# Kernel tuning notes

Hardware: AMD Instinct MI355X
Metric: run time of the kernel (lower is better)

Reference implementation:

```python
import jax, jax.numpy as jnp
import numpy as np

N = 100000   # nodes
E = 1600000  # edges (avg degree 16)
D = 128      # in_dim == hidden_dim
L = 3        # num_layers
LN_EPS = 1e-5


def setup_inputs() -> dict:
    key = jax.random.key(0)
    ks = jax.random.split(key, 4)
    x = jax.random.normal(ks[0], (N, D), dtype=jnp.float32)
    edge_index = jax.random.randint(ks[1], (2, E), 0, N, dtype=jnp.int32)
    s = 1.0 / np.sqrt(D)
    W1 = jax.random.normal(ks[2], (L, D, D), dtype=jnp.float32) * s
    b1 = jnp.zeros((L, D), jnp.float32)
    W2 = jax.random.normal(ks[3], (L, D, D), dtype=jnp.float32) * s
    b2 = jnp.zeros((L, D), jnp.float32)
    gamma = jnp.ones((L, D), jnp.float32)
    beta = jnp.zeros((L, D), jnp.float32)
    return dict(x=x, edge_index=edge_index, W1=W1, b1=b1, W2=W2, b2=b2,
                gamma=gamma, beta=beta)


def _layer_norm(h, g, b):
    mu = jnp.mean(h, axis=-1, keepdims=True)
    var = jnp.mean((h - mu) ** 2, axis=-1, keepdims=True)
    return (h - mu) * jax.lax.rsqrt(var + LN_EPS) * g + b


def reference(x, edge_index, W1, b1, W2, b2, gamma, beta):
    # PyG GINConv (eps=0): mlp(x + sum_{j in N(i)} x_j), messages flow src->dst.
    src, dst = edge_index[0], edge_index[1]
    h = x
    for l in range(L):
        agg = jax.ops.segment_sum(h[src], dst, num_segments=N)  # [N, D]
        z = h + agg                                              # (1+eps)*x + agg, eps=0
        z = jnp.maximum(z @ W1[l] + b1[l], 0.0) @ W2[l] + b2[l]  # 2-layer MLP
        h = jnp.maximum(_layer_norm(z, gamma[l], beta[l]), 0.0)  # LayerNorm + ReLU
        # dropout p=0.0 (eval): identity
    return h
```

## Files before the change

### kernel.cpp

```cpp
#include <hip/hip_runtime.h>

#define NN 100000
#define EE 1600000
#define DD 128
#define LL 3

typedef float f32x4 __attribute__((ext_vector_type(4)));
typedef _Float16 f16x8 __attribute__((ext_vector_type(8)));
typedef unsigned short u16;
typedef unsigned int u32;
typedef u16 u16x8 __attribute__((ext_vector_type(8)));

#define NBUCK ((NN + 255) / 256)
#define CHUNK 16384
#define NCHUNK ((EE + CHUNK - 1) / CHUNK)

__device__ __forceinline__ u16 f2h_bits(float f) {
    _Float16 h = (_Float16)f;
    return __builtin_bit_cast(u16, h);
}
__device__ __forceinline__ float2 h2f2(u32 v) {
    _Float16 lo = __builtin_bit_cast(_Float16, (u16)(v & 0xffff));
    _Float16 hi = __builtin_bit_cast(_Float16, (u16)(v >> 16));
    return make_float2((float)lo, (float)hi);
}
__device__ __forceinline__ u32 f22h(float x, float y) {
    return (u32)f2h_bits(x) | ((u32)f2h_bits(y) << 16);
}


__global__ __launch_bounds__(1024) void csr_hist(const int* __restrict__ dst,
                                                 int* __restrict__ hist_g) {
    __shared__ int h[NBUCK];
    int t = threadIdx.x, c = blockIdx.x;
    for (int i = t; i < NBUCK; i += 1024) h[i] = 0;
    __syncthreads();
    int base = c * CHUNK;
    #pragma unroll
    for (int i = 0; i < CHUNK / 1024; ++i) {
        int e = base + t + i * 1024;
        if (e < EE) atomicAdd(&h[dst[e] >> 8], 1);
    }
    __syncthreads();
    for (int i = t; i < NBUCK; i += 1024) hist_g[i * NCHUNK + c] = h[i];
}

__global__ __launch_bounds__(512) void csr_scan(int* __restrict__ hist_g,
                                                int* __restrict__ bbase) {
    __shared__ int tot[512];
    int t = threadIdx.x;
    int sum = 0;
    if (t < NBUCK) {
        int* p = hist_g + t * NCHUNK;
        for (int c = 0; c < NCHUNK; ++c) { int v = p[c]; p[c] = sum; sum += v; }
    }
    tot[t] = sum; __syncthreads();
    for (int off = 1; off < 512; off <<= 1) {
        int u = (t >= off) ? tot[t - off] : 0;
        __syncthreads();
        tot[t] += u;
        __syncthreads();
    }
    int base = tot[t] - sum;
    if (t < NBUCK) {
        bbase[t] = base;
        int* p = hist_g + t * NCHUNK;
        for (int c = 0; c < NCHUNK; ++c) p[c] += base;
    }
    if (t == 0) bbase[NBUCK] = EE;
}

__global__ __launch_bounds__(1024) void csr_scatter(const int* __restrict__ src,
                                                    const int* __restrict__ dst,
                                                    const int* __restrict__ hist_g,
                                                    u32* __restrict__ rec) {
    __shared__ int cur[NBUCK];
    int t = threadIdx.x, c = blockIdx.x;
    for (int i = t; i < NBUCK; i += 1024) cur[i] = hist_g[i * NCHUNK + c];
    __syncthreads();
    int base = c * CHUNK;
    #pragma unroll
    for (int i = 0; i < CHUNK / 1024; ++i) {
        int e = base + t + i * 1024;
        if (e < EE) {
            int d = dst[e];
            int slot = atomicAdd(&cur[d >> 8], 1);
            rec[slot] = (u32)src[e] | ((u32)(d & 255) << 17);
        }
    }
}

__global__ __launch_bounds__(256) void csr_finalize(const u32* __restrict__ rec,
                                                    const int* __restrict__ bbase,
                                                    int* __restrict__ row_ptr,
                                                    int* __restrict__ col) {
    __shared__ int cur[256];
    __shared__ int sc[256];
    int b = blockIdx.x, t = threadIdx.x;
    int base = bbase[b], tot = bbase[b + 1] - base;
    sc[t] = 0; __syncthreads();
    for (int r = t; r < tot; r += 256) atomicAdd(&sc[rec[base + r] >> 17], 1);
    __syncthreads();
    int v = sc[t];
    for (int off = 1; off < 256; off <<= 1) {
        int u = (t >= off) ? sc[t - off] : 0;
        __syncthreads();
        sc[t] += u;
        __syncthreads();
    }
    int excl = sc[t] - v;
    cur[t] = excl;
    int nid = b * 256 + t;
    if (nid <= NN) row_ptr[nid] = base + excl;
    __syncthreads();
    for (int r = t; r < tot; r += 256) {
        u32 rc = rec[base + r];
        int slot = atomicAdd(&cur[rc >> 17], 1);
        col[base + slot] = (int)(rc & 0x1FFFFu);
    }
}


__global__ void cvt_kernel(const float* __restrict__ x, u32* __restrict__ h) {
    int i = blockIdx.x * blockDim.x + threadIdx.x;
    if (i < NN * 32) {
        float4 v = ((const float4*)x)[i];
        h[i * 2]     = f22h(v.x, v.y);
        h[i * 2 + 1] = f22h(v.z, v.w);
    }
}


__global__ __launch_bounds__(256) void agg16_kernel(
    const u32* __restrict__ h, const int* __restrict__ row_ptr,
    const int* __restrict__ col, u32* __restrict__ z) {
    int node = blockIdx.x * 4 + (threadIdx.x >> 6);
    int c = threadIdx.x & 63;
    const u32* hp = h + c;
    float2 acc = h2f2(hp[(size_t)node * 64]);
    int beg = row_ptr[node], end = row_ptr[node + 1];
    for (int j = beg; j < end; j += 8) {
        int n = end - j;
        u32 v[8];
        #pragma unroll
        for (int q = 0; q < 8; ++q) {
            int jj = (q < n) ? j + q : j;
            v[q] = hp[(size_t)col[jj] * 64];
        }
        #pragma unroll
        for (int q = 0; q < 8; ++q) {
            if (q < n) { float2 f = h2f2(v[q]); acc.x += f.x; acc.y += f.y; }
        }
    }
    z[(size_t)node * 64 + c] = f22h(acc.x, acc.y);
}


__device__ __forceinline__ void stage_w(const float* __restrict__ W, unsigned char* lds, int tid) {
    #pragma unroll
    for (int i = 0; i < 8; ++i) {
        int p = tid + i * 256;
        int c = p & 127;
        int k0 = (p >> 7) << 3;
        u16x8 t;
        #pragma unroll
        for (int j = 0; j < 8; ++j) t[j] = f2h_bits(W[(k0 + j) * 128 + c]);
        u32 off = ((((u32)c << 7) + k0) << 1) ^ (((u32)c & 7) << 4);
        *(u16x8*)(lds + off) = t;
    }
}

__global__ __launch_bounds__(256) void mlp_kernel(
    const u16* __restrict__ z16, const float* __restrict__ W1,
    const float* __restrict__ b1v, const float* __restrict__ W2,
    const float* __restrict__ b2v, const float* __restrict__ gam,
    const float* __restrict__ bet, u16* __restrict__ h16out,
    float* __restrict__ f32out)
{
    __shared__ __align__(16) unsigned char lds[49152];
    const int tid = threadIdx.x;
    const int lane = tid & 63;
    const int w = tid >> 6;
    const int rl = lane & 15;
    const int kg = lane >> 4;
    const int tile = blockIdx.x * 64;
    const int r0 = tile + w * 16;

    stage_w(W1, lds, tid);

    int zrow = r0 + rl; if (zrow > NN - 1) zrow = NN - 1;
    const u16* zp = z16 + (size_t)zrow * 128;
    f16x8 afr[4];
    #pragma unroll
    for (int kt = 0; kt < 4; ++kt)
        afr[kt] = *(const f16x8*)(zp + kt * 32 + kg * 8);
    __syncthreads();

    #pragma unroll
    for (int nt = 0; nt < 8; ++nt) {
        f32x4 acc = {0.f, 0.f, 0.f, 0.f};
        int c = nt * 16 + rl;
        #pragma unroll
        for (int kt = 0; kt < 4; ++kt) {
            int kb = kt * 32 + kg * 8;
            u32 off = ((((u32)c << 7) + kb) << 1) ^ (((u32)c & 7) << 4);
            f16x8 b = *(const f16x8*)(lds + off);
            acc = __builtin_amdgcn_mfma_f32_16x16x32_f16(afr[kt], b, acc, 0, 0, 0);
        }
        float bias = b1v[c];
        #pragma unroll
        for (int r = 0; r < 4; ++r) {
            float v = acc[r] + bias;
            v = v > 0.f ? v : 0.f;
            int fullrow = w * 16 + kg * 4 + r;
            u32 hoff = 32768u + (((((u32)fullrow << 7) + c) << 1) ^ (((u32)fullrow & 7) << 4));
            *(u16*)(lds + hoff) = f2h_bits(v);
        }
    }

    __syncthreads();
    stage_w(W2, lds, tid);

    f16x8 afr2[4];
    int hrow = w * 16 + rl;
    #pragma unroll
    for (int kt = 0; kt < 4; ++kt) {
        int kb = kt * 32 + kg * 8;
        u32 off = 32768u + (((((u32)hrow << 7) + kb) << 1) ^ (((u32)hrow & 7) << 4));
        afr2[kt] = *(const f16x8*)(lds + off);
    }
    __syncthreads();

    f32x4 acc2[8];
    #pragma unroll
    for (int nt = 0; nt < 8; ++nt) {
        f32x4 acc = {0.f, 0.f, 0.f, 0.f};
        int c = nt * 16 + rl;
        #pragma unroll
        for (int kt = 0; kt < 4; ++kt) {
            int kb = kt * 32 + kg * 8;
            u32 off = ((((u32)c << 7) + kb) << 1) ^ (((u32)c & 7) << 4);
            f16x8 b = *(const f16x8*)(lds + off);
            acc = __builtin_amdgcn_mfma_f32_16x16x32_f16(afr2[kt], b, acc, 0, 0, 0);
        }
        float bias = b2v[c];
        acc[0] += bias; acc[1] += bias; acc[2] += bias; acc[3] += bias;
        acc2[nt] = acc;
    }

    float gamv[8], betv[8];
    #pragma unroll
    for (int nt = 0; nt < 8; ++nt) { gamv[nt] = gam[nt * 16 + rl]; betv[nt] = bet[nt * 16 + rl]; }
    #pragma unroll
    for (int r = 0; r < 4; ++r) {
        float s1 = 0.f, s2 = 0.f;
        #pragma unroll
        for (int nt = 0; nt < 8; ++nt) { float v = acc2[nt][r]; s1 += v; s2 += v * v; }
        #pragma unroll
        for (int m = 1; m < 16; m <<= 1) {
            s1 += __shfl_xor(s1, m, 64);
            s2 += __shfl_xor(s2, m, 64);
        }
        float mu = s1 * (1.f / 128.f);
        float var = s2 * (1.f / 128.f) - mu * mu;
        float rstd = rsqrtf(var + 1e-5f);
        int fullrow = r0 + kg * 4 + r;
        if (fullrow < NN) {
            #pragma unroll
            for (int nt = 0; nt < 8; ++nt) {
                float v = (acc2[nt][r] - mu) * rstd * gamv[nt] + betv[nt];
                v = v > 0.f ? v : 0.f;
                if (h16out) h16out[(size_t)fullrow * 128 + nt * 16 + rl] = f2h_bits(v);
                if (f32out) f32out[(size_t)fullrow * 128 + nt * 16 + rl] = v;
            }
        }
    }
}


extern "C" void kernel_launch(void* const* d_in, const int* in_sizes, int n_in,
                              void* d_out, int out_size, void* d_ws, size_t ws_size,
                              hipStream_t stream) {
    const float* x     = (const float*)d_in[0];
    const int*   ei    = (const int*)d_in[1];
    const float* W1    = (const float*)d_in[2];
    const float* b1    = (const float*)d_in[3];
    const float* W2    = (const float*)d_in[4];
    const float* b2    = (const float*)d_in[5];
    const float* gamma = (const float*)d_in[6];
    const float* beta  = (const float*)d_in[7];
    float* out = (float*)d_out;

    const int* src = ei;
    const int* dst = ei + EE;

    unsigned char* ws = (unsigned char*)d_ws;
    size_t off = 0;
    int* hist_g  = (int*)(ws + off); off += (size_t)NBUCK * NCHUNK * 4;
    int* bbase   = (int*)(ws + off); off += (size_t)(NBUCK + 1) * 4;
    int* row_ptr = (int*)(ws + off); off += (size_t)(NN + 1) * 4; off = (off + 255) & ~(size_t)255;
    u32* rec     = (u32*)(ws + off); off += (size_t)EE * 4;       off = (off + 255) & ~(size_t)255;
    int* colv    = (int*)(ws + off); off += (size_t)EE * 4;       off = (off + 255) & ~(size_t)255;
    u32* h16a    = (u32*)(ws + off); off += (size_t)NN * 64 * 4;
    u32* h16b    = (u32*)(ws + off); off += (size_t)NN * 64 * 4;
    u32* z16     = (u32*)(ws + off); off += (size_t)NN * 64 * 4;

    csr_hist<<<NCHUNK, 1024, 0, stream>>>(dst, hist_g);
    csr_scan<<<1, 512, 0, stream>>>(hist_g, bbase);
    csr_scatter<<<NCHUNK, 1024, 0, stream>>>(src, dst, hist_g, rec);
    csr_finalize<<<NBUCK, 256, 0, stream>>>(rec, bbase, row_ptr, colv);
    cvt_kernel<<<(NN * 32 + 255) / 256, 256, 0, stream>>>(x, h16a);

    const u32* hin = h16a;
    u32* hnext = h16b;
    for (int l = 0; l < LL; ++l) {
        agg16_kernel<<<NN / 4, 256, 0, stream>>>(hin, row_ptr, colv, z16);
        mlp_kernel<<<(NN + 63) / 64, 256, 0, stream>>>(
            (const u16*)z16, W1 + (size_t)l * DD * DD, b1 + l * DD,
            W2 + (size_t)l * DD * DD, b2 + l * DD,
            gamma + l * DD, beta + l * DD,
            (l < LL - 1) ? (u16*)hnext : (u16*)nullptr,
            (l == LL - 1) ? out : (float*)nullptr);
        hin = hnext;
        hnext = (hnext == h16a) ? h16b : h16a;
    }
}
```

Measured before the change: 356.4 us.

## Fuse neighbor aggregation into MLP layer kernel via LDS-staged z tile

```diff
diff --git a/kernel.cpp b/kernel.cpp
--- a/kernel.cpp
+++ b/kernel.cpp
@@ -131,31 +131,6 @@
 }
 
 
-__global__ __launch_bounds__(256) void agg16_kernel(
-    const u32* __restrict__ h, const int* __restrict__ row_ptr,
-    const int* __restrict__ col, u32* __restrict__ z) {
-    int node = blockIdx.x * 4 + (threadIdx.x >> 6);
-    int c = threadIdx.x & 63;
-    const u32* hp = h + c;
-    float2 acc = h2f2(hp[(size_t)node * 64]);
-    int beg = row_ptr[node], end = row_ptr[node + 1];
-    for (int j = beg; j < end; j += 8) {
-        int n = end - j;
-        u32 v[8];
-        #pragma unroll
-        for (int q = 0; q < 8; ++q) {
-            int jj = (q < n) ? j + q : j;
-            v[q] = hp[(size_t)col[jj] * 64];
-        }
-        #pragma unroll
-        for (int q = 0; q < 8; ++q) {
-            if (q < n) { float2 f = h2f2(v[q]); acc.x += f.x; acc.y += f.y; }
-        }
-    }
-    z[(size_t)node * 64 + c] = f22h(acc.x, acc.y);
-}
-
-
 __device__ __forceinline__ void stage_w(const float* __restrict__ W, unsigned char* lds, int tid) {
     #pragma unroll
     for (int i = 0; i < 8; ++i) {
@@ -170,12 +145,13 @@
     }
 }
 
-__global__ __launch_bounds__(256) void mlp_kernel(
-    const u16* __restrict__ z16, const float* __restrict__ W1,
-    const float* __restrict__ b1v, const float* __restrict__ W2,
-    const float* __restrict__ b2v, const float* __restrict__ gam,
-    const float* __restrict__ bet, u16* __restrict__ h16out,
-    float* __restrict__ f32out)
+__global__ __launch_bounds__(256) void layer_kernel(
+    const u32* __restrict__ h, const int* __restrict__ row_ptr,
+    const int* __restrict__ col,
+    const float* __restrict__ W1, const float* __restrict__ b1v,
+    const float* __restrict__ W2, const float* __restrict__ b2v,
+    const float* __restrict__ gam, const float* __restrict__ bet,
+    u16* __restrict__ h16out, float* __restrict__ f32out)
 {
     __shared__ __align__(16) unsigned char lds[49152];
     const int tid = threadIdx.x;
@@ -188,12 +164,41 @@
 
     stage_w(W1, lds, tid);
 
-    int zrow = r0 + rl; if (zrow > NN - 1) zrow = NN - 1;
-    const u16* zp = z16 + (size_t)zrow * 128;
+    const u32* hp = h + lane;
+    for (int i = 0; i < 16; ++i) {
+        int r = w * 16 + i;
+        int node = tile + r;
+        float2 acc = make_float2(0.f, 0.f);
+        if (node < NN) {
+            acc = h2f2(hp[(size_t)node * 64]);
+            int beg = row_ptr[node], end = row_ptr[node + 1];
+            for (int j = beg; j < end; j += 8) {
+                int n = end - j;
+                u32 v[8];
+                #pragma unroll
+                for (int q = 0; q < 8; ++q) {
+                    int jj = (q < n) ? j + q : j;
+                    v[q] = hp[(size_t)col[jj] * 64];
+                }
+                #pragma unroll
+                for (int q = 0; q < 8; ++q) {
+                    if (q < n) { float2 f = h2f2(v[q]); acc.x += f.x; acc.y += f.y; }
+                }
+            }
+        }
+        u32 zoff = 32768u + ((((u32)r << 8) + ((u32)lane << 2)) ^ (((u32)r & 7) << 4));
+        *(u32*)(lds + zoff) = f22h(acc.x, acc.y);
+    }
+
     f16x8 afr[4];
-    #pragma unroll
-    for (int kt = 0; kt < 4; ++kt)
-        afr[kt] = *(const f16x8*)(zp + kt * 32 + kg * 8);
+    {
+        int zr = w * 16 + rl;
+        #pragma unroll
+        for (int kt = 0; kt < 4; ++kt) {
+            u32 off = 32768u + ((((u32)zr << 8) + (u32)(kt * 64 + kg * 16)) ^ (((u32)zr & 7) << 4));
+            afr[kt] = *(const f16x8*)(lds + off);
+        }
+    }
     __syncthreads();
 
     #pragma unroll
@@ -303,7 +308,6 @@
     int* colv    = (int*)(ws + off); off += (size_t)EE * 4;       off = (off + 255) & ~(size_t)255;
     u32* h16a    = (u32*)(ws + off); off += (size_t)NN * 64 * 4;
     u32* h16b    = (u32*)(ws + off); off += (size_t)NN * 64 * 4;
-    u32* z16     = (u32*)(ws + off); off += (size_t)NN * 64 * 4;
 
     csr_hist<<<NCHUNK, 1024, 0, stream>>>(dst, hist_g);
     csr_scan<<<1, 512, 0, stream>>>(hist_g, bbase);
@@ -314,9 +318,9 @@
     const u32* hin = h16a;
     u32* hnext = h16b;
     for (int l = 0; l < LL; ++l) {
-        agg16_kernel<<<NN / 4, 256, 0, stream>>>(hin, row_ptr, colv, z16);
-        mlp_kernel<<<(NN + 63) / 64, 256, 0, stream>>>(
-            (const u16*)z16, W1 + (size_t)l * DD * DD, b1 + l * DD,
+        layer_kernel<<<(NN + 63) / 64, 256, 0, stream>>>(
+            hin, row_ptr, colv,
+            W1 + (size_t)l * DD * DD, b1 + l * DD,
             W2 + (size_t)l * DD * DD, b2 + l * DD,
             gamma + l * DD, beta + l * DD,
             (l < LL - 1) ? (u16*)hnext : (u16*)nullptr,
```

New measurement: 587.8 us. 64.9% more time.

## Pad CSR rows to multiples of eight with zero sentinel node, use packed fp16 adds

Applied to the files above, without the earlier changes.

```diff
diff --git a/kernel.cpp b/kernel.cpp
--- a/kernel.cpp
+++ b/kernel.cpp
@@ -7,6 +7,7 @@
 
 typedef float f32x4 __attribute__((ext_vector_type(4)));
 typedef _Float16 f16x8 __attribute__((ext_vector_type(8)));
+typedef _Float16 f16x2 __attribute__((ext_vector_type(2)));
 typedef unsigned short u16;
 typedef unsigned int u32;
 typedef u16 u16x8 __attribute__((ext_vector_type(8)));
@@ -14,15 +15,14 @@
 #define NBUCK ((NN + 255) / 256)
 #define CHUNK 16384
 #define NCHUNK ((EE + CHUNK - 1) / CHUNK)
+#define PADMAX 1792
 
 __device__ __forceinline__ u16 f2h_bits(float f) {
     _Float16 h = (_Float16)f;
     return __builtin_bit_cast(u16, h);
 }
-__device__ __forceinline__ float2 h2f2(u32 v) {
-    _Float16 lo = __builtin_bit_cast(_Float16, (u16)(v & 0xffff));
-    _Float16 hi = __builtin_bit_cast(_Float16, (u16)(v >> 16));
-    return make_float2((float)lo, (float)hi);
+__device__ __forceinline__ f16x2 bc16x2(u32 v) {
+    return __builtin_bit_cast(f16x2, v);
 }
 __device__ __forceinline__ u32 f22h(float x, float y) {
     return (u32)f2h_bits(x) | ((u32)f2h_bits(y) << 16);
@@ -92,31 +92,36 @@
 
 __global__ __launch_bounds__(256) void csr_finalize(const u32* __restrict__ rec,
                                                     const int* __restrict__ bbase,
-                                                    int* __restrict__ row_ptr,
+                                                    int* __restrict__ rbeg,
+                                                    int* __restrict__ rpend,
                                                     int* __restrict__ col) {
     __shared__ int cur[256];
     __shared__ int sc[256];
     int b = blockIdx.x, t = threadIdx.x;
     int base = bbase[b], tot = bbase[b + 1] - base;
+    int pbase = base + b * PADMAX;
     sc[t] = 0; __syncthreads();
     for (int r = t; r < tot; r += 256) atomicAdd(&sc[rec[base + r] >> 17], 1);
     __syncthreads();
-    int v = sc[t];
+    int cnt = sc[t];
+    int pcnt = (cnt + 7) & ~7;
+    sc[t] = pcnt; __syncthreads();
     for (int off = 1; off < 256; off <<= 1) {
         int u = (t >= off) ? sc[t - off] : 0;
         __syncthreads();
         sc[t] += u;
         __syncthreads();
     }
-    int excl = sc[t] - v;
-    cur[t] = excl;
+    int mybeg = pbase + sc[t] - pcnt;
+    cur[t] = mybeg;
     int nid = b * 256 + t;
-    if (nid <= NN) row_ptr[nid] = base + excl;
+    if (nid < NN) { rbeg[nid] = mybeg; rpend[nid] = mybeg + pcnt; }
+    for (int k = cnt; k < pcnt; ++k) col[mybeg + k] = NN;
     __syncthreads();
     for (int r = t; r < tot; r += 256) {
         u32 rc = rec[base + r];
         int slot = atomicAdd(&cur[rc >> 17], 1);
-        col[base + slot] = (int)(rc & 0x1FFFFu);
+        col[slot] = (int)(rc & 0x1FFFFu);
     }
 }
 
@@ -132,27 +137,27 @@
 
 
 __global__ __launch_bounds__(256) void agg16_kernel(
-    const u32* __restrict__ h, const int* __restrict__ row_ptr,
-    const int* __restrict__ col, u32* __restrict__ z) {
+    const u32* __restrict__ h, const int* __restrict__ rbeg,
+    const int* __restrict__ rpend, const int* __restrict__ col,
+    u32* __restrict__ z) {
     int node = blockIdx.x * 4 + (threadIdx.x >> 6);
     int c = threadIdx.x & 63;
     const u32* hp = h + c;
-    float2 acc = h2f2(hp[(size_t)node * 64]);
-    int beg = row_ptr[node], end = row_ptr[node + 1];
+    f16x2 self = bc16x2(hp[(size_t)node * 64]);
+    float accx = (float)self[0], accy = (float)self[1];
+    int beg = rbeg[node], end = rpend[node];
     for (int j = beg; j < end; j += 8) {
-        int n = end - j;
         u32 v[8];
         #pragma unroll
-        for (int q = 0; q < 8; ++q) {
-            int jj = (q < n) ? j + q : j;
-            v[q] = hp[(size_t)col[jj] * 64];
-        }
-        #pragma unroll
-        for (int q = 0; q < 8; ++q) {
-            if (q < n) { float2 f = h2f2(v[q]); acc.x += f.x; acc.y += f.y; }
-        }
-    }
-    z[(size_t)node * 64 + c] = f22h(acc.x, acc.y);
+        for (int q = 0; q < 8; ++q) v[q] = hp[(size_t)col[j + q] * 64];
+        f16x2 s0 = bc16x2(v[0]) + bc16x2(v[1]);
+        f16x2 s1 = bc16x2(v[2]) + bc16x2(v[3]);
+        f16x2 s2 = bc16x2(v[4]) + bc16x2(v[5]);
+        f16x2 s3 = bc16x2(v[6]) + bc16x2(v[7]);
+        s0 = s0 + s1; s2 = s2 + s3; s0 = s0 + s2;
+        accx += (float)s0[0]; accy += (float)s0[1];
+    }
+    z[(size_t)node * 64 + c] = f22h(accx, accy);
 }
 
 
@@ -298,23 +303,27 @@
     size_t off = 0;
     int* hist_g  = (int*)(ws + off); off += (size_t)NBUCK * NCHUNK * 4;
     int* bbase   = (int*)(ws + off); off += (size_t)(NBUCK + 1) * 4;
-    int* row_ptr = (int*)(ws + off); off += (size_t)(NN + 1) * 4; off = (off + 255) & ~(size_t)255;
-    u32* rec     = (u32*)(ws + off); off += (size_t)EE * 4;       off = (off + 255) & ~(size_t)255;
-    int* colv    = (int*)(ws + off); off += (size_t)EE * 4;       off = (off + 255) & ~(size_t)255;
-    u32* h16a    = (u32*)(ws + off); off += (size_t)NN * 64 * 4;
-    u32* h16b    = (u32*)(ws + off); off += (size_t)NN * 64 * 4;
+    int* rbeg    = (int*)(ws + off); off += (size_t)NN * 4;
+    int* rpend   = (int*)(ws + off); off += (size_t)NN * 4; off = (off + 255) & ~(size_t)255;
+    u32* rec     = (u32*)(ws + off); off += (size_t)EE * 4; off = (off + 255) & ~(size_t)255;
+    int* colv    = (int*)(ws + off); off += ((size_t)EE + (size_t)NBUCK * PADMAX + 64) * 4;
+    off = (off + 255) & ~(size_t)255;
+    u32* h16a    = (u32*)(ws + off); off += (size_t)(NN + 1) * 64 * 4;
+    u32* h16b    = (u32*)(ws + off); off += (size_t)(NN + 1) * 64 * 4;
     u32* z16     = (u32*)(ws + off); off += (size_t)NN * 64 * 4;
 
     csr_hist<<<NCHUNK, 1024, 0, stream>>>(dst, hist_g);
     csr_scan<<<1, 512, 0, stream>>>(hist_g, bbase);
     csr_scatter<<<NCHUNK, 1024, 0, stream>>>(src, dst, hist_g, rec);
-    csr_finalize<<<NBUCK, 256, 0, stream>>>(rec, bbase, row_ptr, colv);
+    csr_finalize<<<NBUCK, 256, 0, stream>>>(rec, bbase, rbeg, rpend, colv);
     cvt_kernel<<<(NN * 32 + 255) / 256, 256, 0, stream>>>(x, h16a);
+    hipMemsetAsync(h16a + (size_t)NN * 64, 0, 256, stream);
+    hipMemsetAsync(h16b + (size_t)NN * 64, 0, 256, stream);
 
     const u32* hin = h16a;
     u32* hnext = h16b;
     for (int l = 0; l < LL; ++l) {
-        agg16_kernel<<<NN / 4, 256, 0, stream>>>(hin, row_ptr, colv, z16);
+        agg16_kernel<<<NN / 4, 256, 0, stream>>>(hin, rbeg, rpend, colv, z16);
         mlp_kernel<<<(NN + 63) / 64, 256, 0, stream>>>(
             (const u16*)z16, W1 + (size_t)l * DD * DD, b1 + l * DD,
             W2 + (size_t)l * DD * DD, b2 + l * DD,
```

Measured after the change: 342.7 us. -3.8%, faster.
